# Kernel optimization log

Hardware: AMD Instinct MI355X
Metric: run time of the kernel (lower is better)

The kernel has to match this reference:

```python
import jax, jax.numpy as jnp
import numpy as np

N = 50000   # num points (pts_x1 == pts_x2, as when pts_x2 is None)
C = 64      # flattened leading dims of u (size_nm1)
K = 48      # max neighbors per epsilon-ball (padding cap)
EPS = 0.015 # epsilon ball radius; ~pi*eps^2*N ~ 35 expected neighbors


def _build_neighbors(pts, eps, k):
    """Brute-force epsilon-ball query (replaces cKDTree.query_ball_point),
    returning fixed-K padded neighbor indices + validity mask."""
    n = pts.shape[0]
    nb_idx = np.zeros((n, k), dtype=np.int32)
    nb_mask = np.zeros((n, k), dtype=bool)
    sq = (pts * pts).sum(-1)
    eps2 = eps * eps
    chunk = 1000
    for s in range(0, n, chunk):
        e = min(s + chunk, n)
        # squared distances [chunk, n] via ||a||^2 + ||b||^2 - 2 a.b
        d2 = sq[s:e, None] + sq[None, :] - 2.0 * (pts[s:e] @ pts.T)
        within = d2 <= eps2  # each point includes itself (d2 ~ 0)
        # stable sort: in-ball indices first, in ascending index order
        order = np.argsort(~within, axis=1, kind='stable')[:, :k]
        counts = np.minimum(within.sum(axis=1), k)
        nb_idx[s:e] = order.astype(np.int32)
        nb_mask[s:e] = np.arange(k)[None, :] < counts[:, None]
    # padded slots point at index 0 but are masked out
    nb_idx[~nb_mask] = 0
    return nb_idx, nb_mask


def setup_inputs() -> dict:
    rng = np.random.default_rng(0)
    pts = rng.random((N, 2)).astype(np.float32)          # pts_x1 == pts_x2
    u = rng.standard_normal((C, N)).astype(np.float32)   # uj values
    nb_idx, nb_mask = _build_neighbors(pts, EPS, K)
    return {
        "u": jnp.asarray(u),
        "pts_x2": jnp.asarray(pts),
        "neighbor_idx": jnp.asarray(nb_idx),
        "neighbor_mask": jnp.asarray(nb_mask),
    }


def reference(u, pts_x2, neighbor_idx, neighbor_mask):
    # v[c, i] = max_{j in N_i(eps)} u[c, j]
    uu = u[:, neighbor_idx]                               # [C, N2, K] gather
    neg_inf = jnp.asarray(-jnp.inf, dtype=u.dtype)
    uu = jnp.where(neighbor_mask[None, :, :], uu, neg_inf)
    ui = jnp.max(uu, axis=-1)                             # [C, N2]
    return ui, pts_x2
```

## Files before the change

kernel.cpp:

```cpp
#include <hip/hip_runtime.h>
#include <hip/hip_fp16.h>
#include <math.h>


__device__ __forceinline__ unsigned int pkmax(unsigned int a, unsigned int b) {
    unsigned int r;
    asm("v_pk_max_f16 %0, %1, %2" : "=v"(r) : "v"(a), "v"(b));
    return r;
}

__device__ __forceinline__ float h2f_lo(unsigned int x) {
    return __half2float(__ushort_as_half((unsigned short)(x & 0xffffu)));
}
__device__ __forceinline__ float h2f_hi(unsigned int x) {
    return __half2float(__ushort_as_half((unsigned short)(x >> 16)));
}

__global__ __launch_bounds__(256) void transpose_u_kernel(
    const float* __restrict__ u, unsigned int* __restrict__ uht32,
    const float* __restrict__ pts, float* __restrict__ pts_out, int n)
{
    __shared__ float tile[64 * 65];
    const int tid   = threadIdx.x;
    const int ibase = blockIdx.x * 64;

    {
        const int il = tid & 63;
        const int cq = tid >> 6;
        const int i  = ibase + il;
        #pragma unroll
        for (int pass = 0; pass < 16; ++pass) {
            const int c = cq + pass * 4;
            tile[c * 65 + il] = (i < n) ? u[(size_t)c * n + i] : 0.0f;
        }
    }
    __syncthreads();
    {
        const int l = tid & 31;
        const int r = tid >> 5;
        #pragma unroll
        for (int pass = 0; pass < 8; ++pass) {
            const int ir = r + pass * 8;
            const int i  = ibase + ir;
            if (i < n) {
                const unsigned short h0 = __half_as_ushort(__float2half(tile[(2 * l + 0) * 65 + ir]));
                const unsigned short h1 = __half_as_ushort(__float2half(tile[(2 * l + 1) * 65 + ir]));
                uht32[(size_t)i * 32 + l] = (unsigned int)h0 | ((unsigned int)h1 << 16);
            }
        }
    }
    const int gid = blockIdx.x * 256 + tid;
    if (gid < 2 * n) pts_out[gid] = pts[gid];
}

#define WAVES 8
__global__ __launch_bounds__(512, 4) void maxpool_kernel(
    const unsigned short* __restrict__ uht,
    const int* __restrict__ nb_idx,
    float* __restrict__ out, int n)
{
    __shared__ int   s_idxT[WAVES][48 * 9];
    __shared__ float s_out[64 * 65];

    const int tid   = threadIdx.x;
    const int w     = tid >> 6;
    const int lane  = tid & 63;
    const int ibase = blockIdx.x * 64;
    const int pbase = w * 8;

    int maxcnt = 1;
    #pragma unroll
    for (int ps = 0; ps < 8; ++ps) {
        const int i = ibase + pbase + ps;
        int jv = 0;
        if (i < n && lane < 48) jv = nb_idx[(size_t)i * 48 + lane];
        const bool inval = (lane >= 48) || (lane > 0 && jv == 0);
        const unsigned long long m = __ballot(inval);
        const int cnt = (int)__builtin_ctzll(m);
        const int j0  = __shfl(jv, 0);
        if (lane < 48) s_idxT[w][lane * 9 + ps] = (lane < cnt) ? jv : j0;
        maxcnt = max(maxcnt, cnt);
    }

    const int p8 = lane >> 3;
    const int c8 = lane & 7;
    const char* ub = (const char*)uht;
    const size_t coff = (size_t)(c8 << 4);
    const int* idxw = s_idxT[w];

    unsigned int a0 = 0xFC00FC00u;
    unsigned int a1 = a0, a2 = a0, a3 = a0;

#define BODY(J)                                                              \
    {                                                                        \
        const int idv = idxw[(J) * 9 + p8];                                  \
        const uint4 d = *(const uint4*)(ub + ((size_t)(unsigned)idv << 7) + coff); \
        a0 = pkmax(a0, d.x);                                                 \
        a1 = pkmax(a1, d.y);                                                 \
        a2 = pkmax(a2, d.z);                                                 \
        a3 = pkmax(a3, d.w);                                                 \
    }

    const int mc4 = (maxcnt + 3) & ~3;
    for (int j = 0; j < mc4; j += 4) {
        BODY(j) BODY(j + 1) BODY(j + 2) BODY(j + 3)
    }
#undef BODY

    {
        float* dst = &s_out[(pbase + p8) * 65 + c8 * 8];
        dst[0] = h2f_lo(a0); dst[1] = h2f_hi(a0);
        dst[2] = h2f_lo(a1); dst[3] = h2f_hi(a1);
        dst[4] = h2f_lo(a2); dst[5] = h2f_hi(a2);
        dst[6] = h2f_lo(a3); dst[7] = h2f_hi(a3);
    }
    __syncthreads();

    const int nv = min(64, n - ibase);
    #pragma unroll
    for (int r = 0; r < 8; ++r) {
        const int c = w * 8 + r;
        if (lane < nv) out[(size_t)c * n + ibase + lane] = s_out[lane * 65 + c];
    }
}

extern "C" void kernel_launch(void* const* d_in, const int* in_sizes, int n_in,
                              void* d_out, int out_size, void* d_ws, size_t ws_size,
                              hipStream_t stream)
{
    const float* u   = (const float*)d_in[0];
    const float* pts = (const float*)d_in[1];
    const int*   nb  = (const int*)d_in[2];
    float* out = (float*)d_out;

    const int n = in_sizes[1] / 2;
    const int c = in_sizes[0] / n;

    unsigned int* uht = (unsigned int*)d_ws;
    const int nblk = (n + 63) / 64;

    transpose_u_kernel<<<nblk, 256, 0, stream>>>(u, uht, pts, out + (size_t)c * n, n);
    maxpool_kernel<<<nblk, 512, 0, stream>>>((const unsigned short*)d_ws, nb, out, n);
}
```

Baseline: 37.25 us.

## Split fp16 transposed table into channel halves and gather per-half blocks

The transposed fp16 table is split into two planes holding channels 0-31 and 32-63, so each row becomes 64 bytes instead of 128. The max-pool kernel now runs 256-thread blocks over 32 points each, and block IDs are interleaved so that four tiles of one channel half run together. Each lane gathers 8-byte pieces instead of 16-byte ones, which shrinks the working set per plane and should improve cache hit rates for the random neighbor gathers. In exchange, the neighbor index rows are loaded twice (once per half), the gathers are narrower, and there are more blocks.

Result: slower. 43.27 us (+16.2%).

```diff
diff --git a/kernel.cpp b/kernel.cpp
--- a/kernel.cpp
+++ b/kernel.cpp
@@ -8,7 +8,6 @@
     asm("v_pk_max_f16 %0, %1, %2" : "=v"(r) : "v"(a), "v"(b));
     return r;
 }
-
 __device__ __forceinline__ float h2f_lo(unsigned int x) {
     return __half2float(__ushort_as_half((unsigned short)(x & 0xffffu)));
 }
@@ -17,7 +16,8 @@
 }
 
 __global__ __launch_bounds__(256) void transpose_u_kernel(
-    const float* __restrict__ u, unsigned int* __restrict__ uht32,
+    const float* __restrict__ u,
+    unsigned int* __restrict__ lo32, unsigned int* __restrict__ hi32,
     const float* __restrict__ pts, float* __restrict__ pts_out, int n)
 {
     __shared__ float tile[64 * 65];
@@ -45,7 +45,9 @@
             if (i < n) {
                 const unsigned short h0 = __half_as_ushort(__float2half(tile[(2 * l + 0) * 65 + ir]));
                 const unsigned short h1 = __half_as_ushort(__float2half(tile[(2 * l + 1) * 65 + ir]));
-                uht32[(size_t)i * 32 + l] = (unsigned int)h0 | ((unsigned int)h1 << 16);
+                const unsigned int word = (unsigned int)h0 | ((unsigned int)h1 << 16);
+                if (l < 16) lo32[(size_t)i * 16 + l]        = word;
+                else        hi32[(size_t)i * 16 + (l - 16)] = word;
             }
         }
     }
@@ -53,19 +55,26 @@
     if (gid < 2 * n) pts_out[gid] = pts[gid];
 }
 
-#define WAVES 8
-__global__ __launch_bounds__(512, 4) void maxpool_kernel(
-    const unsigned short* __restrict__ uht,
+#define NW 4
+__global__ __launch_bounds__(256, 6) void maxpool_kernel(
+    const unsigned short* __restrict__ ulo,
+    const unsigned short* __restrict__ uhi,
     const int* __restrict__ nb_idx,
-    float* __restrict__ out, int n)
+    float* __restrict__ out, int n, int ntiles)
 {
-    __shared__ int   s_idxT[WAVES][48 * 9];
-    __shared__ float s_out[64 * 65];
+    const int bid  = blockIdx.x;
+    const int sub  = bid & 7;
+    const int pass = (sub >= 4) ? 1 : 0;
+    const int tile = (bid >> 3) * 4 + (sub & 3);
+    if (tile >= ntiles) return;
+    const int ibase = tile * 32;
+
+    __shared__ int   s_idxT[NW][48 * 9];
+    __shared__ float s_out[32 * 36];
 
     const int tid   = threadIdx.x;
     const int w     = tid >> 6;
     const int lane  = tid & 63;
-    const int ibase = blockIdx.x * 64;
     const int pbase = w * 8;
 
     int maxcnt = 1;
@@ -84,43 +93,42 @@
 
     const int p8 = lane >> 3;
     const int c8 = lane & 7;
-    const char* ub = (const char*)uht;
-    const size_t coff = (size_t)(c8 << 4);
+    const char* ub = (const char*)(pass ? uhi : ulo);
+    const unsigned coff = (unsigned)(c8 << 3);
     const int* idxw = s_idxT[w];
 
     unsigned int a0 = 0xFC00FC00u;
-    unsigned int a1 = a0, a2 = a0, a3 = a0;
+    unsigned int a1 = 0xFC00FC00u;
 
-#define BODY(J)                                                              \
-    {                                                                        \
-        const int idv = idxw[(J) * 9 + p8];                                  \
-        const uint4 d = *(const uint4*)(ub + ((size_t)(unsigned)idv << 7) + coff); \
-        a0 = pkmax(a0, d.x);                                                 \
-        a1 = pkmax(a1, d.y);                                                 \
-        a2 = pkmax(a2, d.z);                                                 \
-        a3 = pkmax(a3, d.w);                                                 \
+#define BODY(J)                                                               \
+    {                                                                         \
+        const int idv = idxw[(J) * 9 + p8];                                   \
+        const unsigned off = ((unsigned)idv << 6) + coff;                     \
+        const uint2 d = *(const uint2*)(ub + off);                            \
+        a0 = pkmax(a0, d.x);                                                  \
+        a1 = pkmax(a1, d.y);                                                  \
     }
 
-    const int mc4 = (maxcnt + 3) & ~3;
-    for (int j = 0; j < mc4; j += 4) {
-        BODY(j) BODY(j + 1) BODY(j + 2) BODY(j + 3)
+    const int mc8 = (maxcnt + 7) & ~7;
+    for (int j = 0; j < mc8; j += 8) {
+        BODY(j)     BODY(j + 1) BODY(j + 2) BODY(j + 3)
+        BODY(j + 4) BODY(j + 5) BODY(j + 6) BODY(j + 7)
     }
 #undef BODY
 
     {
-        float* dst = &s_out[(pbase + p8) * 65 + c8 * 8];
+        float* dst = &s_out[(pbase + p8) * 36 + c8 * 4];
         dst[0] = h2f_lo(a0); dst[1] = h2f_hi(a0);
         dst[2] = h2f_lo(a1); dst[3] = h2f_hi(a1);
-        dst[4] = h2f_lo(a2); dst[5] = h2f_hi(a2);
-        dst[6] = h2f_lo(a3); dst[7] = h2f_hi(a3);
     }
     __syncthreads();
 
-    const int nv = min(64, n - ibase);
+    const int nv = min(32, n - ibase);
     #pragma unroll
     for (int r = 0; r < 8; ++r) {
-        const int c = w * 8 + r;
-        if (lane < nv) out[(size_t)c * n + ibase + lane] = s_out[lane * 65 + c];
+        const int cl = w * 8 + r;
+        const int c  = pass * 32 + cl;
+        if (lane < nv) out[(size_t)c * n + ibase + lane] = s_out[lane * 36 + cl];
     }
 }
 
@@ -136,9 +144,14 @@
     const int n = in_sizes[1] / 2;
     const int c = in_sizes[0] / n;
 
-    unsigned int* uht = (unsigned int*)d_ws;
-    const int nblk = (n + 63) / 64;
+    unsigned short* ulo = (unsigned short*)d_ws;
+    unsigned short* uhi = ulo + (size_t)n * 32;
 
-    transpose_u_kernel<<<nblk, 256, 0, stream>>>(u, uht, pts, out + (size_t)c * n, n);
-    maxpool_kernel<<<nblk, 512, 0, stream>>>((const unsigned short*)d_ws, nb, out, n);
+    const int nblk_t = (n + 63) / 64;
+    const int ntiles = (n + 31) / 32;
+    const int nblk_m = ((ntiles + 3) / 4) * 8;
+
+    transpose_u_kernel<<<nblk_t, 256, 0, stream>>>(
+        u, (unsigned int*)ulo, (unsigned int*)uhi, pts, out + (size_t)c * n, n);
+    maxpool_kernel<<<nblk_m, 256, 0, stream>>>(ulo, uhi, nb, out, n, ntiles);
 }
```

## Reorder points by spatial grid cells to improve gather locality

Applied to the files above, without the earlier changes.

Adds a counting sort of points into a 64x64 spatial grid (histogram, scan, scatter). The fp16 transposed u table is written in the sorted order, the max-gather runs over sorted points with remapped neighbor indices, and a final pass un-permutes the results into the output. The aim is to make neighbor gathers hit nearby rows so cache reuse improves. In exchange it adds five extra launches plus a memset, atomics, and an extra round trip through an intermediate output buffer. The sorted position is stored in 16 bits, which only works while n fits in 65536.

Result: slower. 58.99 us (+58.4%).

```diff
diff --git a/kernel.cpp b/kernel.cpp
--- a/kernel.cpp
+++ b/kernel.cpp
@@ -2,23 +2,83 @@
 #include <hip/hip_fp16.h>
 #include <math.h>
 
+
+#define NCELLS 4096
 
 __device__ __forceinline__ unsigned int pkmax(unsigned int a, unsigned int b) {
     unsigned int r;
     asm("v_pk_max_f16 %0, %1, %2" : "=v"(r) : "v"(a), "v"(b));
     return r;
 }
-
 __device__ __forceinline__ float h2f_lo(unsigned int x) {
     return __half2float(__ushort_as_half((unsigned short)(x & 0xffffu)));
 }
 __device__ __forceinline__ float h2f_hi(unsigned int x) {
     return __half2float(__ushort_as_half((unsigned short)(x >> 16)));
 }
-
-__global__ __launch_bounds__(256) void transpose_u_kernel(
-    const float* __restrict__ u, unsigned int* __restrict__ uht32,
-    const float* __restrict__ pts, float* __restrict__ pts_out, int n)
+__device__ __forceinline__ int cell_of(float2 p) {
+    int cx = (int)(p.x * 64.0f); cx = cx < 0 ? 0 : (cx > 63 ? 63 : cx);
+    int cy = (int)(p.y * 64.0f); cy = cy < 0 ? 0 : (cy > 63 ? 63 : cy);
+    return cy * 64 + cx;
+}
+
+__global__ __launch_bounds__(256) void hist_kernel(
+    const float2* __restrict__ pts, unsigned* __restrict__ cnt, int n)
+{
+    const int i = blockIdx.x * 256 + threadIdx.x;
+    if (i < n) atomicAdd(&cnt[cell_of(pts[i])], 1u);
+}
+
+__global__ __launch_bounds__(1024) void scan_kernel(
+    const unsigned* __restrict__ cnt, unsigned* __restrict__ base,
+    unsigned* __restrict__ cur)
+{
+    const int tid  = threadIdx.x;
+    const int lane = tid & 63;
+    const uint4 c  = ((const uint4*)cnt)[tid];
+    ((uint4*)cur)[tid] = make_uint4(0u, 0u, 0u, 0u);
+    const unsigned s = c.x + c.y + c.z + c.w;
+
+    unsigned v = s;
+    #pragma unroll
+    for (int d = 1; d < 64; d <<= 1) {
+        const unsigned t = __shfl_up(v, d);
+        if (lane >= d) v += t;
+    }
+    __shared__ unsigned sW[16];
+    if (lane == 63) sW[tid >> 6] = v;
+    __syncthreads();
+    if (tid == 0) {
+        unsigned run = 0;
+        #pragma unroll
+        for (int t = 0; t < 16; ++t) { const unsigned w0 = sW[t]; sW[t] = run; run += w0; }
+    }
+    __syncthreads();
+    const unsigned incl = v + sW[tid >> 6];
+    const unsigned excl = incl - s;
+    uint4 b;
+    b.x = excl; b.y = b.x + c.x; b.z = b.y + c.y; b.w = b.z + c.z;
+    ((uint4*)base)[tid] = b;
+}
+
+__global__ __launch_bounds__(256) void scatter_kernel(
+    const float2* __restrict__ pts, const unsigned* __restrict__ base,
+    unsigned* __restrict__ cur, int* __restrict__ perm,
+    unsigned short* __restrict__ inv16, int n)
+{
+    const int i = blockIdx.x * 256 + threadIdx.x;
+    if (i < n) {
+        const int cell = cell_of(pts[i]);
+        const unsigned pos = base[cell] + atomicAdd(&cur[cell], 1u);
+        perm[pos] = i;
+        inv16[i]  = (unsigned short)pos;
+    }
+}
+
+__global__ __launch_bounds__(256) void transpose_kernel(
+    const float* __restrict__ u, const unsigned short* __restrict__ inv16,
+    unsigned int* __restrict__ us32, const float* __restrict__ pts,
+    float* __restrict__ pts_out, int n)
 {
     __shared__ float tile[64 * 65];
     const int tid   = threadIdx.x;
@@ -30,8 +90,8 @@
         const int i  = ibase + il;
         #pragma unroll
         for (int pass = 0; pass < 16; ++pass) {
-            const int c = cq + pass * 4;
-            tile[c * 65 + il] = (i < n) ? u[(size_t)c * n + i] : 0.0f;
+            const int ch = cq + pass * 4;
+            tile[ch * 65 + il] = (i < n) ? u[(size_t)ch * n + i] : 0.0f;
         }
     }
     __syncthreads();
@@ -45,7 +105,7 @@
             if (i < n) {
                 const unsigned short h0 = __half_as_ushort(__float2half(tile[(2 * l + 0) * 65 + ir]));
                 const unsigned short h1 = __half_as_ushort(__float2half(tile[(2 * l + 1) * 65 + ir]));
-                uht32[(size_t)i * 32 + l] = (unsigned int)h0 | ((unsigned int)h1 << 16);
+                us32[(size_t)inv16[i] * 32 + l] = (unsigned int)h0 | ((unsigned int)h1 << 16);
             }
         }
     }
@@ -53,74 +113,103 @@
     if (gid < 2 * n) pts_out[gid] = pts[gid];
 }
 
-#define WAVES 8
-__global__ __launch_bounds__(512, 4) void maxpool_kernel(
-    const unsigned short* __restrict__ uht,
-    const int* __restrict__ nb_idx,
+__global__ __launch_bounds__(512) void gather_kernel(
+    const unsigned short* __restrict__ us,
+    const int* __restrict__ nb,
+    const int* __restrict__ perm,
+    const unsigned short* __restrict__ inv16,
+    unsigned int* __restrict__ outs,
+    int n)
+{
+    __shared__ int s_idx[48 * 65];
+
+    const int tid   = threadIdx.x;
+    const int w     = tid >> 6;
+    const int lane  = tid & 63;
+    const int pbase = blockIdx.x * 64;
+
+    int maxcnt = 1;
+    #pragma unroll
+    for (int ps = 0; ps < 8; ++ps) {
+        const int p   = w * 8 + ps;
+        const int pos = pbase + p;
+        int jv = 0;
+        if (pos < n) {
+            const int iorig = perm[pos];
+            if (lane < 48) jv = nb[(size_t)iorig * 48 + lane];
+        }
+        const bool inval = (lane >= 48) || (lane > 0 && jv == 0);
+        const unsigned long long m = __ballot(inval);
+        const int cnt = (int)__builtin_ctzll(m);
+        const int jt  = (int)inv16[jv];
+        const int t0  = __shfl(jt, 0);
+        if (lane < 48) s_idx[lane * 65 + p] = (lane < cnt) ? jt : t0;
+        maxcnt = max(maxcnt, cnt);
+    }
+
+    const int p   = w * 8 + (lane >> 3);
+    const int c8  = lane & 7;
+    const char* ub = (const char*)us;
+    const unsigned coff = (unsigned)(c8 << 4);
+
+    unsigned int a0 = 0xFC00FC00u;
+    unsigned int a1 = a0, a2 = a0, a3 = a0;
+
+#define BODY(J)                                                               \
+    {                                                                         \
+        const unsigned idv = (unsigned)s_idx[(J) * 65 + p];                   \
+        const uint4 d = *(const uint4*)(ub + (((size_t)idv << 7) + coff));    \
+        a0 = pkmax(a0, d.x);                                                  \
+        a1 = pkmax(a1, d.y);                                                  \
+        a2 = pkmax(a2, d.z);                                                  \
+        a3 = pkmax(a3, d.w);                                                  \
+    }
+
+    const int mc8 = (maxcnt + 7) & ~7;
+    for (int j = 0; j < mc8; j += 8) {
+        BODY(j)     BODY(j + 1) BODY(j + 2) BODY(j + 3)
+        BODY(j + 4) BODY(j + 5) BODY(j + 6) BODY(j + 7)
+    }
+#undef BODY
+
+    const int pos = pbase + p;
+    if (pos < n) {
+        unsigned int* dst = outs + (size_t)pos * 32 + c8 * 4;
+        dst[0] = a0; dst[1] = a1; dst[2] = a2; dst[3] = a3;
+    }
+}
+
+__global__ __launch_bounds__(256) void unperm_kernel(
+    const unsigned int* __restrict__ outs, const unsigned short* __restrict__ inv16,
     float* __restrict__ out, int n)
 {
-    __shared__ int   s_idxT[WAVES][48 * 9];
-    __shared__ float s_out[64 * 65];
-
+    __shared__ float s_t[64 * 65];
     const int tid   = threadIdx.x;
     const int w     = tid >> 6;
     const int lane  = tid & 63;
     const int ibase = blockIdx.x * 64;
-    const int pbase = w * 8;
-
-    int maxcnt = 1;
-    #pragma unroll
-    for (int ps = 0; ps < 8; ++ps) {
-        const int i = ibase + pbase + ps;
-        int jv = 0;
-        if (i < n && lane < 48) jv = nb_idx[(size_t)i * 48 + lane];
-        const bool inval = (lane >= 48) || (lane > 0 && jv == 0);
-        const unsigned long long m = __ballot(inval);
-        const int cnt = (int)__builtin_ctzll(m);
-        const int j0  = __shfl(jv, 0);
-        if (lane < 48) s_idxT[w][lane * 9 + ps] = (lane < cnt) ? jv : j0;
-        maxcnt = max(maxcnt, cnt);
-    }
-
     const int p8 = lane >> 3;
     const int c8 = lane & 7;
-    const char* ub = (const char*)uht;
-    const size_t coff = (size_t)(c8 << 4);
-    const int* idxw = s_idxT[w];
-
-    unsigned int a0 = 0xFC00FC00u;
-    unsigned int a1 = a0, a2 = a0, a3 = a0;
-
-#define BODY(J)                                                              \
-    {                                                                        \
-        const int idv = idxw[(J) * 9 + p8];                                  \
-        const uint4 d = *(const uint4*)(ub + ((size_t)(unsigned)idv << 7) + coff); \
-        a0 = pkmax(a0, d.x);                                                 \
-        a1 = pkmax(a1, d.y);                                                 \
-        a2 = pkmax(a2, d.z);                                                 \
-        a3 = pkmax(a3, d.w);                                                 \
-    }
-
-    const int mc4 = (maxcnt + 3) & ~3;
-    for (int j = 0; j < mc4; j += 4) {
-        BODY(j) BODY(j + 1) BODY(j + 2) BODY(j + 3)
-    }
-#undef BODY
-
-    {
-        float* dst = &s_out[(pbase + p8) * 65 + c8 * 8];
-        dst[0] = h2f_lo(a0); dst[1] = h2f_hi(a0);
-        dst[2] = h2f_lo(a1); dst[3] = h2f_hi(a1);
-        dst[4] = h2f_lo(a2); dst[5] = h2f_hi(a2);
-        dst[6] = h2f_lo(a3); dst[7] = h2f_hi(a3);
+
+    #pragma unroll
+    for (int pass = 0; pass < 2; ++pass) {
+        const int p = pass * 32 + w * 8 + p8;
+        const int i = ibase + p;
+        const unsigned row = (i < n) ? (unsigned)inv16[i] : 0u;
+        const uint4 d = *(const uint4*)(outs + (size_t)row * 32 + c8 * 4);
+        float* dst = &s_t[p * 65 + c8 * 8];
+        dst[0] = h2f_lo(d.x); dst[1] = h2f_hi(d.x);
+        dst[2] = h2f_lo(d.y); dst[3] = h2f_hi(d.y);
+        dst[4] = h2f_lo(d.z); dst[5] = h2f_hi(d.z);
+        dst[6] = h2f_lo(d.w); dst[7] = h2f_hi(d.w);
     }
     __syncthreads();
 
     const int nv = min(64, n - ibase);
     #pragma unroll
-    for (int r = 0; r < 8; ++r) {
-        const int c = w * 8 + r;
-        if (lane < nv) out[(size_t)c * n + ibase + lane] = s_out[lane * 65 + c];
+    for (int r = 0; r < 16; ++r) {
+        const int c = w * 16 + r;
+        if (lane < nv) out[(size_t)c * n + ibase + lane] = s_t[lane * 65 + c];
     }
 }
 
@@ -136,9 +225,24 @@
     const int n = in_sizes[1] / 2;
     const int c = in_sizes[0] / n;
 
-    unsigned int* uht = (unsigned int*)d_ws;
-    const int nblk = (n + 63) / 64;
-
-    transpose_u_kernel<<<nblk, 256, 0, stream>>>(u, uht, pts, out + (size_t)c * n, n);
-    maxpool_kernel<<<nblk, 512, 0, stream>>>((const unsigned short*)d_ws, nb, out, n);
-}
+    char* ws = (char*)d_ws;
+    unsigned*       cnt   = (unsigned*)(ws + 0);
+    unsigned*       base  = (unsigned*)(ws + 16384);
+    unsigned*       cur   = (unsigned*)(ws + 32768);
+    int*            perm  = (int*)(ws + 49152);
+    unsigned short* inv16 = (unsigned short*)(ws + 262144);
+    unsigned short* us    = (unsigned short*)(ws + 524288);
+    unsigned int*   outs  = (unsigned int*)(ws + 8388608);
+
+    const int nb256 = (n + 255) / 256;
+    const int nb64  = (n + 63) / 64;
+
+    hipMemsetAsync(cnt, 0, NCELLS * 4, stream);
+    hist_kernel<<<nb256, 256, 0, stream>>>((const float2*)pts, cnt, n);
+    scan_kernel<<<1, 1024, 0, stream>>>(cnt, base, cur);
+    scatter_kernel<<<nb256, 256, 0, stream>>>((const float2*)pts, base, cur, perm, inv16, n);
+    transpose_kernel<<<nb64, 256, 0, stream>>>(u, inv16, (unsigned int*)us, pts,
+                                               out + (size_t)c * n, n);
+    gather_kernel<<<nb64, 512, 0, stream>>>(us, nb, perm, inv16, outs, n);
+    unperm_kernel<<<nb64, 256, 0, stream>>>(outs, inv16, out, n);
+}
```
